# Kernel tuning notes

Hardware: AMD Instinct MI355X
Metric: run time of the kernel (lower is better)

Reference implementation:

```python
import jax, jax.numpy as jnp
import numpy as np

N_NODES = 100000
N_EDGES = 1600000
IN_C, HID_C, OUT_C = 128, 128, 64


def setup_inputs() -> dict:
    key = jax.random.key(0)
    ks = jax.random.split(key, 8)
    x = jax.random.normal(ks[0], (N_NODES, IN_C), dtype=jnp.float32)
    edge_index = jax.random.randint(ks[1], (2, N_EDGES), 0, N_NODES, dtype=jnp.int32)
    # Glorot-ish init for GCNConv linear weights, zero bias (PyG default)
    def glorot(k, fan_in, fan_out):
        s = jnp.sqrt(6.0 / (fan_in + fan_out))
        return jax.random.uniform(k, (fan_in, fan_out), dtype=jnp.float32, minval=-s, maxval=s)
    return {
        "x": x,
        "edge_index": edge_index,
        "W1": glorot(ks[2], IN_C, HID_C), "b1": jnp.zeros((HID_C,), jnp.float32),
        "W2": glorot(ks[3], HID_C, HID_C), "b2": jnp.zeros((HID_C,), jnp.float32),
        "W3": glorot(ks[4], HID_C, OUT_C), "b3": jnp.zeros((OUT_C,), jnp.float32),
    }


def _gcn_norm(edge_index, num_nodes):
    # Add self-loops (PyG GCNConv default) and compute symmetric normalization
    loops = jnp.arange(num_nodes, dtype=edge_index.dtype)
    src = jnp.concatenate([edge_index[0], loops])  # [E+N]
    dst = jnp.concatenate([edge_index[1], loops])
    deg = jax.ops.segment_sum(jnp.ones_like(dst, dtype=jnp.float32), dst,
                              num_segments=num_nodes)
    deg_inv_sqrt = jnp.where(deg > 0, jax.lax.rsqrt(jnp.maximum(deg, 1.0)), 0.0)
    norm = deg_inv_sqrt[src] * deg_inv_sqrt[dst]  # [E+N]
    return src, dst, norm


def _gcn_layer(x, src, dst, norm, W, b, num_nodes):
    h = x @ W                                # [N, out] dense transform first
    msg = h[src] * norm[:, None]             # gather + scale  [E+N, out]
    out = jax.ops.segment_sum(msg, dst, num_segments=num_nodes)  # scatter-add
    return out + b


def reference(x, edge_index, W1, b1, W2, b2, W3, b3):
    n = x.shape[0]
    src, dst, norm = _gcn_norm(edge_index, n)
    h = jax.nn.relu(_gcn_layer(x, src, dst, norm, W1, b1, n))
    h = jax.nn.relu(_gcn_layer(h, src, dst, norm, W2, b2, n))
    return _gcn_layer(h, src, dst, norm, W3, b3, n)
```

## Files before the change

### kernel.cpp

```cpp
#include <hip/hip_runtime.h>

#define NN 100000
#define NE 1600000
#define NBK 391
#define BSH 8
#define MPAD 100096
#define SCB 391
#define CAP 5120
#define NB16 6250

typedef unsigned short ushortT;
typedef unsigned long long ull;
using sh8 = __attribute__((ext_vector_type(8))) short;
using f4  = __attribute__((ext_vector_type(4))) float;


__device__ __forceinline__ unsigned short bfr(float f) {
  unsigned u = __float_as_uint(f);
  u += 0x7FFF + ((u >> 16) & 1);
  return (unsigned short)(u >> 16);
}
__device__ __forceinline__ float bf2f(unsigned short h) {
  return __uint_as_float(((unsigned)h) << 16);
}
__device__ __forceinline__ void acc8(const uint4 v, float* a) {
  a[0] += __uint_as_float(v.x << 16);
  a[1] += __uint_as_float(v.x & 0xFFFF0000u);
  a[2] += __uint_as_float(v.y << 16);
  a[3] += __uint_as_float(v.y & 0xFFFF0000u);
  a[4] += __uint_as_float(v.z << 16);
  a[5] += __uint_as_float(v.z & 0xFFFF0000u);
  a[6] += __uint_as_float(v.w << 16);
  a[7] += __uint_as_float(v.w & 0xFFFF0000u);
}
__device__ __forceinline__ sh8 hi8(const float4 a, const float4 b) {
  sh8 r;
  r[0] = (short)bfr(a.x); r[1] = (short)bfr(a.y);
  r[2] = (short)bfr(a.z); r[3] = (short)bfr(a.w);
  r[4] = (short)bfr(b.x); r[5] = (short)bfr(b.y);
  r[6] = (short)bfr(b.z); r[7] = (short)bfr(b.w);
  return r;
}


template <int COUT>
__device__ __forceinline__ void packone(const float* __restrict__ W,
                                        ushortT* __restrict__ Bp, int i) {
  const int j = i & 7;
  const int l = (i >> 3) & 63;
  const int rest = i >> 9;
  const int g = rest % (COUT / 16);
  const int ks = rest / (COUT / 16);
  const int k = (ks & 3) * 32 + (l >> 4) * 8 + j;
  const int n = g * 16 + (l & 15);
  const float v = W[k * COUT + n];
  const unsigned short h = bfr(v);
  Bp[i] = (ks < 4) ? h : bfr(v - bf2f(h));
}


__global__ __launch_bounds__(256) void k_scatterpack(
    const int* __restrict__ src, const int* __restrict__ dst,
    int* __restrict__ cursor, unsigned* __restrict__ pairArr,
    const float* __restrict__ W1, const float* __restrict__ W2,
    const float* __restrict__ W3, ushortT* __restrict__ Bp1,
    ushortT* __restrict__ Bp2, ushortT* __restrict__ Bp3) {
  if (blockIdx.x >= SCB) {
    const int i = (blockIdx.x - SCB) * 256 + threadIdx.x;
    if (i < 32768) packone<128>(W1, Bp1, i);
    else if (i < 65536) packone<128>(W2, Bp2, i - 32768);
    else packone<64>(W3, Bp3, i - 65536);
    return;
  }
  __shared__ int lcnt[512];
  __shared__ int lbase[512];
  __shared__ int lrank[NBK];
  __shared__ int bbase[NBK];
  __shared__ int sd2[256];
  __shared__ unsigned sorted[4096];
  __shared__ int target[4096];
  const int t = threadIdx.x;
  for (int i = t; i < 512; i += 256) lcnt[i] = 0;
  for (int i = t; i < NBK; i += 256) lrank[i] = 0;
  __syncthreads();
  const int base = blockIdx.x * 4096;
  int rs[16], rd[16];
#pragma unroll
  for (int q = 0; q < 16; q++) {
    int e = base + t + 256 * q;
    rs[q] = (e < NE) ? src[e] : -1;
    rd[q] = (e < NE) ? dst[e] : -1;
    if (rd[q] >= 0) atomicAdd(&lcnt[rd[q] >> BSH], 1);
  }
  __syncthreads();
  const int s0 = lcnt[2 * t];
  const int s1 = lcnt[2 * t + 1];
  sd2[t] = s0 + s1;
  __syncthreads();
  for (int off = 1; off < 256; off <<= 1) {
    int x = (t >= off) ? sd2[t - off] : 0;
    __syncthreads();
    sd2[t] += x;
    __syncthreads();
  }
  const int epair = sd2[t] - (s0 + s1);
  lbase[2 * t] = epair;
  lbase[2 * t + 1] = epair + s0;
  __syncthreads();
  for (int i = t; i < NBK; i += 256)
    if (lcnt[i] > 0) bbase[i] = atomicAdd(&cursor[i], lcnt[i]);
  __syncthreads();
#pragma unroll
  for (int q = 0; q < 16; q++) {
    if (rd[q] >= 0) {
      int b = rd[q] >> BSH;
      int r = atomicAdd(&lrank[b], 1);
      int slot = lbase[b] + r;
      sorted[slot] = ((unsigned)rs[q] << 8) | ((unsigned)rd[q] & 255u);
      target[slot] = b * CAP + bbase[b] + r;
    }
  }
  __syncthreads();
  const int n = min(4096, NE - base);
  for (int s = t; s < n; s += 256) pairArr[target[s]] = sorted[s];
}


__global__ __launch_bounds__(256) void k_buildcsr(const unsigned* __restrict__ pairArr,
                                                  const int* __restrict__ cnt,
                                                  float* __restrict__ dinv,
                                                  int* __restrict__ rowptr,
                                                  int* __restrict__ col) {
  __shared__ int lc[256];
  __shared__ int sd[256];
  __shared__ int bc[NBK];
  const int t = threadIdx.x;
  const int b = blockIdx.x;
  const int n0 = b << BSH;
  for (int i = t; i < NBK; i += 256) bc[i] = cnt[i];
  lc[t] = 0;
  __syncthreads();
  int partial = 0;
  for (int i = t; i < b; i += 256) partial += bc[i];
  sd[t] = partial;
  __syncthreads();
  for (int off = 128; off > 0; off >>= 1) {
    if (t < off) sd[t] += sd[t + off];
    __syncthreads();
  }
  const int ebeg = sd[0];
  const int myCnt = bc[b];
  __syncthreads();
  const unsigned* pb = pairArr + (size_t)b * CAP;
  for (int i = t; i < myCnt; i += 256)
    atomicAdd(&lc[pb[i] & 255u], 1);
  __syncthreads();
  const int v = lc[t];
  sd[t] = v;
  __syncthreads();
  for (int off = 1; off < 256; off <<= 1) {
    int x = (t >= off) ? sd[t - off] : 0;
    __syncthreads();
    sd[t] += x;
    __syncthreads();
  }
  const int excl = sd[t] - v;
  lc[t] = excl;
  const int node = n0 + t;
  if (node < NN) {
    rowptr[node] = ebeg + excl;
    dinv[node] = rsqrtf(1.0f + (float)v);
  }
  if (b == 0 && t == 0) rowptr[NN] = NE;
  __syncthreads();
  for (int i = t; i < myCnt; i += 256) {
    unsigned p = pb[i];
    int d = (int)(p & 255u);
    int srcv = (int)(p >> 8);
    int pos = atomicAdd(&lc[d], 1);
    col[ebeg + pos] = srcv;
  }
}


template <int COUT, bool FUSED>
__global__ __launch_bounds__(256) void k_gemmM(const ushortT* __restrict__ A,
                                               const float* __restrict__ X,
                                               const ushortT* __restrict__ Bp,
                                               const float* __restrict__ dinv,
                                               ushortT* __restrict__ hs) {
  constexpr int CGALL = COUT / 16;
  constexpr int RG = 2;
  constexpr int CG = 4;
  const int w = threadIdx.x >> 6;
  const int lane = threadIdx.x & 63;
  const int q = lane >> 4;
  const int c = lane & 15;
  int row0, cg0;
  if (COUT == 128) {
    row0 = blockIdx.x * 64 + (w & 1) * 32;
    cg0 = (w >> 1) * 4;
  } else {
    row0 = blockIdx.x * 128 + w * 32;
    cg0 = 0;
  }

  const ushortT* ap[RG];
  const float* xp[RG];
#pragma unroll
  for (int rg = 0; rg < RG; rg++) {
    const int row = row0 + rg * 16 + c;
    if (FUSED) xp[rg] = X + (size_t)min(row, NN - 1) * 128 + q * 8;
    else ap[rg] = A + (size_t)row * 128 + q * 8;
  }
  const ushortT* bp0 = Bp + (size_t)lane * 8;

  f4 acc[RG][CG];
#pragma unroll
  for (int i = 0; i < RG; i++)
#pragma unroll
    for (int j = 0; j < CG; j++) acc[i][j] = (f4){0.f, 0.f, 0.f, 0.f};

  sh8 ah[RG], bh[CG], bl[CG];
  sh8 nah[RG], nbh[CG], nbl[CG];

  auto loadA = [&](int kr, sh8 (&h)[RG]) {
#pragma unroll
    for (int rg = 0; rg < RG; rg++) {
      if (FUSED) {
        const float4 x0 = *reinterpret_cast<const float4*>(xp[rg] + kr * 32);
        const float4 x1 = *reinterpret_cast<const float4*>(xp[rg] + kr * 32 + 4);
        h[rg] = hi8(x0, x1);
      } else {
        h[rg] = *reinterpret_cast<const sh8*>(ap[rg] + kr * 32);
      }
    }
  };
  auto loadB = [&](int kr, sh8 (&h)[CG], sh8 (&l)[CG]) {
#pragma unroll
    for (int cg = 0; cg < CG; cg++) {
      h[cg] = *reinterpret_cast<const sh8*>(bp0 + (size_t)(kr * CGALL + cg0 + cg) * 512);
      l[cg] = *reinterpret_cast<const sh8*>(bp0 + (size_t)((4 + kr) * CGALL + cg0 + cg) * 512);
    }
  };

  loadA(0, ah);
  loadB(0, bh, bl);
#pragma unroll
  for (int kr = 0; kr < 4; kr++) {
    if (kr < 3) {
      loadA(kr + 1, nah);
      loadB(kr + 1, nbh, nbl);
    }
#pragma unroll
    for (int rg = 0; rg < RG; rg++)
#pragma unroll
      for (int cg = 0; cg < CG; cg++)
        acc[rg][cg] = __builtin_amdgcn_mfma_f32_16x16x32_bf16(ah[rg], bh[cg],
                                                              acc[rg][cg], 0, 0, 0);
#pragma unroll
    for (int rg = 0; rg < RG; rg++)
#pragma unroll
      for (int cg = 0; cg < CG; cg++)
        acc[rg][cg] = __builtin_amdgcn_mfma_f32_16x16x32_bf16(ah[rg], bl[cg],
                                                              acc[rg][cg], 0, 0, 0);
    if (kr < 3) {
#pragma unroll
      for (int rg = 0; rg < RG; rg++) ah[rg] = nah[rg];
#pragma unroll
      for (int cg = 0; cg < CG; cg++) { bh[cg] = nbh[cg]; bl[cg] = nbl[cg]; }
    }
  }

#pragma unroll
  for (int rg = 0; rg < RG; rg++) {
#pragma unroll
    for (int reg = 0; reg < 4; reg++) {
      const int row = row0 + rg * 16 + q * 4 + reg;
      if (row < NN) {
        const float dv = dinv[row];
#pragma unroll
        for (int cg = 0; cg < CG; cg++) {
          hs[(size_t)row * COUT + (cg0 + cg) * 16 + c] = bfr(acc[rg][cg][reg] * dv);
        }
      }
    }
  }
}


template <int COUT>
__global__ __launch_bounds__(256, 8) void k_aggemm(
    const ushortT* __restrict__ hs_in, const int* __restrict__ rowptr,
    const int* __restrict__ col, const float* __restrict__ dinv,
    const float* __restrict__ bias, const ushortT* __restrict__ Bp,
    ushortT* __restrict__ hs_out) {
  constexpr int CGALL = COUT / 16;
  constexpr int UPW = CGALL / 4;
  __shared__ ushortT At[16 * 128];
  const int t = threadIdx.x;
  const int w = t >> 6;
  const int lane = t & 63;
  const int q = lane >> 4;
  const int c = lane & 15;
  const int chb = c * 8;
  const int n0 = blockIdx.x * 16;
  const int nw0 = n0 + w * 4;

  const int rpv = rowptr[min(nw0 + (lane & 7), NN)];
  const float dvv = dinv[min(nw0 + (lane & 3), NN - 1)];
  const float4 b0 = *reinterpret_cast<const float4*>(bias + chb);
  const float4 b1 = *reinterpret_cast<const float4*>(bias + chb + 4);

  for (int it = 0; it < 4; ++it) {
    const int node = nw0 + it;
    const int r = w * 4 + it;
    const int beg = __shfl(rpv, it);
    const int end = __shfl(rpv, it + 1);
    const float di = __shfl(dvv, it);
    float a[8] = {};
    if (q == 0) {
      const uint4 v = *reinterpret_cast<const uint4*>(hs_in + (long)node * 128 + chb);
      acc8(v, a);
    }
    int j = beg;
    if (j + 8 <= end) {
      int c0 = col[j + q];
      int c1 = col[j + 4 + q];
      while (true) {
        const uint4 v0 = *reinterpret_cast<const uint4*>(hs_in + (long)c0 * 128 + chb);
        const uint4 v1 = *reinterpret_cast<const uint4*>(hs_in + (long)c1 * 128 + chb);
        j += 8;
        const bool more = (j + 8 <= end);
        int m0, m1;
        if (more) { m0 = col[j + q]; m1 = col[j + 4 + q]; }
        acc8(v0, a);
        acc8(v1, a);
        if (!more) break;
        c0 = m0; c1 = m1;
      }
    }
    if (j + 4 <= end) {
      int cc = col[j + q];
      const uint4 v = *reinterpret_cast<const uint4*>(hs_in + (long)cc * 128 + chb);
      acc8(v, a);
      j += 4;
    }
    {
      const int rem = end - j;
      if (q < rem) {
        int cc = col[j + q];
        const uint4 v = *reinterpret_cast<const uint4*>(hs_in + (long)cc * 128 + chb);
        acc8(v, a);
      }
    }
#pragma unroll
    for (int i = 0; i < 8; i++) a[i] += __shfl(a[i], lane ^ 32);
#pragma unroll
    for (int i = 0; i < 8; i++) a[i] += __shfl(a[i], lane ^ 16);
    if (q == 0) {
      float o[8];
      o[0] = fmaf(a[0], di, b0.x); o[1] = fmaf(a[1], di, b0.y);
      o[2] = fmaf(a[2], di, b0.z); o[3] = fmaf(a[3], di, b0.w);
      o[4] = fmaf(a[4], di, b1.x); o[5] = fmaf(a[5], di, b1.y);
      o[6] = fmaf(a[6], di, b1.z); o[7] = fmaf(a[7], di, b1.w);
#pragma unroll
      for (int i = 0; i < 8; i++) o[i] = fmaxf(o[i], 0.f);
      uint4 H;
      H.x = (unsigned)bfr(o[0]) | ((unsigned)bfr(o[1]) << 16);
      H.y = (unsigned)bfr(o[2]) | ((unsigned)bfr(o[3]) << 16);
      H.z = (unsigned)bfr(o[4]) | ((unsigned)bfr(o[5]) << 16);
      H.w = (unsigned)bfr(o[6]) | ((unsigned)bfr(o[7]) << 16);
      const unsigned bo = (unsigned)(r * 256 + c * 16) ^ (unsigned)((r & 7) << 4);
      *reinterpret_cast<uint4*>(reinterpret_cast<char*>(At) + bo) = H;
    }
  }
  __syncthreads();

  const int cg0 = w * UPW;
  const ushortT* bp0 = Bp + (size_t)lane * 8;
  const char* ab = reinterpret_cast<const char*>(At);
  const int arow = c;
  f4 acc[UPW];
#pragma unroll
  for (int u = 0; u < UPW; ++u) acc[u] = (f4){0.f, 0.f, 0.f, 0.f};
#pragma unroll
  for (int kr = 0; kr < 4; ++kr) {
    const unsigned bo =
        (unsigned)(arow * 256 + kr * 64 + q * 16) ^ (unsigned)((arow & 7) << 4);
    const sh8 af = *reinterpret_cast<const sh8*>(ab + bo);
#pragma unroll
    for (int u = 0; u < UPW; ++u) {
      const sh8 bh = *reinterpret_cast<const sh8*>(
          bp0 + (size_t)(kr * CGALL + cg0 + u) * 512);
      acc[u] = __builtin_amdgcn_mfma_f32_16x16x32_bf16(af, bh, acc[u], 0, 0, 0);
    }
#pragma unroll
    for (int u = 0; u < UPW; ++u) {
      const sh8 bl = *reinterpret_cast<const sh8*>(
          bp0 + (size_t)((4 + kr) * CGALL + cg0 + u) * 512);
      acc[u] = __builtin_amdgcn_mfma_f32_16x16x32_bf16(af, bl, acc[u], 0, 0, 0);
    }
  }
#pragma unroll
  for (int reg = 0; reg < 4; ++reg) {
    const int row = n0 + q * 4 + reg;
    const float dv = dinv[row];
#pragma unroll
    for (int u = 0; u < UPW; ++u) {
      hs_out[(size_t)row * COUT + (cg0 + u) * 16 + c] = bfr(acc[u][reg] * dv);
    }
  }
}


__global__ __launch_bounds__(256) void k_agg64(const ushortT* __restrict__ hs,
                                               const int* __restrict__ rowptr,
                                               const int* __restrict__ col,
                                               const float* __restrict__ dinv,
                                               const float* __restrict__ bias,
                                               float* __restrict__ out) {
  const int gid = blockIdx.x * 256 + threadIdx.x;
  const int node = gid >> 6;
  if (node >= NN) return;
  const int lane = threadIdx.x & 63;
  const int o8 = lane >> 3;
  const int chb = (lane & 7) * 8;
  const int beg = rowptr[node];
  const int end = rowptr[node + 1];

  float a[8] = {};
  if (o8 == 0) {
    const uint4 v = *reinterpret_cast<const uint4*>(hs + (long)node * 64 + chb);
    acc8(v, a);
  }

  int j = beg;
  if (j + 16 <= end) {
    int c0 = col[j + o8];
    int c1 = col[j + 8 + o8];
    while (true) {
      const uint4 v0 = *reinterpret_cast<const uint4*>(hs + (long)c0 * 64 + chb);
      const uint4 v1 = *reinterpret_cast<const uint4*>(hs + (long)c1 * 64 + chb);
      j += 16;
      const bool more = (j + 16 <= end);
      int n0, n1;
      if (more) { n0 = col[j + o8]; n1 = col[j + 8 + o8]; }
      acc8(v0, a);
      acc8(v1, a);
      if (!more) break;
      c0 = n0; c1 = n1;
    }
  }
  for (; j + 8 <= end; j += 8) {
    int c = col[j + o8];
    const uint4 v = *reinterpret_cast<const uint4*>(hs + (long)c * 64 + chb);
    acc8(v, a);
  }
  {
    const int r = end - j;
    if (o8 < r) {
      int c = col[j + o8];
      const uint4 v = *reinterpret_cast<const uint4*>(hs + (long)c * 64 + chb);
      acc8(v, a);
    }
  }

#pragma unroll
  for (int i = 0; i < 8; i++) a[i] += __shfl(a[i], lane ^ 32);
#pragma unroll
  for (int i = 0; i < 8; i++) a[i] += __shfl(a[i], lane ^ 16);
#pragma unroll
  for (int i = 0; i < 8; i++) a[i] += __shfl(a[i], lane ^ 8);

  if (o8 == 0) {
    const float di = dinv[node];
    const float4 b0 = *reinterpret_cast<const float4*>(bias + chb);
    const float4 b1 = *reinterpret_cast<const float4*>(bias + chb + 4);
    float4 r0, r1;
    r0.x = fmaf(a[0], di, b0.x); r0.y = fmaf(a[1], di, b0.y);
    r0.z = fmaf(a[2], di, b0.z); r0.w = fmaf(a[3], di, b0.w);
    r1.x = fmaf(a[4], di, b1.x); r1.y = fmaf(a[5], di, b1.y);
    r1.z = fmaf(a[6], di, b1.z); r1.w = fmaf(a[7], di, b1.w);
    *reinterpret_cast<float4*>(out + (long)node * 64 + chb) = r0;
    *reinterpret_cast<float4*>(out + (long)node * 64 + chb + 4) = r1;
  }
}


extern "C" void kernel_launch(void* const* d_in, const int* in_sizes, int n_in,
                              void* d_out, int out_size, void* d_ws, size_t ws_size,
                              hipStream_t stream) {
  const float* x  = (const float*)d_in[0];
  const int* ei   = (const int*)d_in[1];
  const float* W1 = (const float*)d_in[2];
  const float* b1 = (const float*)d_in[3];
  const float* W2 = (const float*)d_in[4];
  const float* b2 = (const float*)d_in[5];
  const float* W3 = (const float*)d_in[6];
  const float* b3 = (const float*)d_in[7];
  float* out = (float*)d_out;
  const int* srcp = ei;
  const int* dstp = ei + NE;

  char* wsb = (char*)d_ws;
  size_t off = 0;
  auto alloc = [&](size_t bytes) -> void* {
    void* p = wsb + off;
    off += (bytes + 255) & ~(size_t)255;
    return p;
  };
  ushortT* hs1 = (ushortT*)alloc((size_t)MPAD * 128 * 2);
  ushortT* hs2 = (ushortT*)alloc((size_t)NN * 128 * 2);
  int*   col    = (int*)alloc((size_t)NE * 4);
  int*   rowptr = (int*)alloc((size_t)(NN + 1) * 4);
  float* dinv   = (float*)alloc((size_t)NN * 4);
  int*   cursor = (int*)alloc((size_t)NBK * 4);
  ushortT* Bp1 = (ushortT*)alloc((size_t)32768 * 2);
  ushortT* Bp2 = (ushortT*)alloc((size_t)32768 * 2);
  ushortT* Bp3 = (ushortT*)alloc((size_t)16384 * 2);
  unsigned* pairArr = (unsigned*)hs2;
  ushortT* hs3 = hs1;
  (void)ws_size; (void)in_sizes; (void)n_in; (void)out_size;

  hipMemsetAsync(cursor, 0, (size_t)NBK * 4, stream);
  k_scatterpack<<<SCB + 320, 256, 0, stream>>>(srcp, dstp, cursor, pairArr,
                                               W1, W2, W3, Bp1, Bp2, Bp3);
  k_buildcsr<<<NBK, 256, 0, stream>>>(pairArr, cursor, dinv, rowptr, col);

  const int aggGrid = (NN * 64) / 256;
  const int gemmGrid128 = MPAD / 64;

  k_gemmM<128, true><<<gemmGrid128, 256, 0, stream>>>(nullptr, x, Bp1, dinv, hs1);
  k_aggemm<128><<<NB16, 256, 0, stream>>>(hs1, rowptr, col, dinv, b1, Bp2, hs2);
  k_aggemm<64><<<NB16, 256, 0, stream>>>(hs2, rowptr, col, dinv, b2, Bp3, hs3);
  k_agg64<<<aggGrid, 256, 0, stream>>>(hs3, rowptr, col, dinv, b3, out);
}
```

Baseline: 350.8 us.

## Replace bucketed two-pass CSR build with global degree histogram, scan, and atomic fill

Replaces the bucket-sort CSR construction (local sort into fixed-capacity buckets, then a per-bucket counting sort) with three kernels: a global atomic degree histogram, a block-wise prefix scan producing rowptr, cursor and dinv, and a per-edge atomic fill of col. This is simpler and drops the pairArr staging buffer. In exchange it relies on 1.6M global atomics on random addresses twice, and col order within a row becomes nondeterministic, which can scatter gather locality. The scan kernel also rereads the degree prefix for each block, doing quadratic work.

```diff
diff --git a/kernel.cpp b/kernel.cpp
--- a/kernel.cpp
+++ b/kernel.cpp
@@ -2,12 +2,11 @@
 
 #define NN 100000
 #define NE 1600000
-#define NBK 391
-#define BSH 8
 #define MPAD 100096
-#define SCB 391
-#define CAP 5120
 #define NB16 6250
+#define HB 1563
+#define FB 6250
+#define SB 98
 
 typedef unsigned short ushortT;
 typedef unsigned long long ull;
@@ -59,127 +58,73 @@
 }
 
 
-__global__ __launch_bounds__(256) void k_scatterpack(
-    const int* __restrict__ src, const int* __restrict__ dst,
-    int* __restrict__ cursor, unsigned* __restrict__ pairArr,
+__global__ __launch_bounds__(256) void k_histpack(
+    const int* __restrict__ dst, int* __restrict__ deg,
     const float* __restrict__ W1, const float* __restrict__ W2,
     const float* __restrict__ W3, ushortT* __restrict__ Bp1,
     ushortT* __restrict__ Bp2, ushortT* __restrict__ Bp3) {
-  if (blockIdx.x >= SCB) {
-    const int i = (blockIdx.x - SCB) * 256 + threadIdx.x;
+  if (blockIdx.x >= HB) {
+    const int i = (blockIdx.x - HB) * 256 + threadIdx.x;
     if (i < 32768) packone<128>(W1, Bp1, i);
     else if (i < 65536) packone<128>(W2, Bp2, i - 32768);
     else packone<64>(W3, Bp3, i - 65536);
     return;
   }
-  __shared__ int lcnt[512];
-  __shared__ int lbase[512];
-  __shared__ int lrank[NBK];
-  __shared__ int bbase[NBK];
-  __shared__ int sd2[256];
-  __shared__ unsigned sorted[4096];
-  __shared__ int target[4096];
-  const int t = threadIdx.x;
-  for (int i = t; i < 512; i += 256) lcnt[i] = 0;
-  for (int i = t; i < NBK; i += 256) lrank[i] = 0;
-  __syncthreads();
-  const int base = blockIdx.x * 4096;
-  int rs[16], rd[16];
-#pragma unroll
-  for (int q = 0; q < 16; q++) {
-    int e = base + t + 256 * q;
-    rs[q] = (e < NE) ? src[e] : -1;
-    rd[q] = (e < NE) ? dst[e] : -1;
-    if (rd[q] >= 0) atomicAdd(&lcnt[rd[q] >> BSH], 1);
-  }
-  __syncthreads();
-  const int s0 = lcnt[2 * t];
-  const int s1 = lcnt[2 * t + 1];
-  sd2[t] = s0 + s1;
-  __syncthreads();
-  for (int off = 1; off < 256; off <<= 1) {
-    int x = (t >= off) ? sd2[t - off] : 0;
-    __syncthreads();
-    sd2[t] += x;
-    __syncthreads();
-  }
-  const int epair = sd2[t] - (s0 + s1);
-  lbase[2 * t] = epair;
-  lbase[2 * t + 1] = epair + s0;
-  __syncthreads();
-  for (int i = t; i < NBK; i += 256)
-    if (lcnt[i] > 0) bbase[i] = atomicAdd(&cursor[i], lcnt[i]);
-  __syncthreads();
-#pragma unroll
-  for (int q = 0; q < 16; q++) {
-    if (rd[q] >= 0) {
-      int b = rd[q] >> BSH;
-      int r = atomicAdd(&lrank[b], 1);
-      int slot = lbase[b] + r;
-      sorted[slot] = ((unsigned)rs[q] << 8) | ((unsigned)rd[q] & 255u);
-      target[slot] = b * CAP + bbase[b] + r;
-    }
-  }
-  __syncthreads();
-  const int n = min(4096, NE - base);
-  for (int s = t; s < n; s += 256) pairArr[target[s]] = sorted[s];
-}
-
-
-__global__ __launch_bounds__(256) void k_buildcsr(const unsigned* __restrict__ pairArr,
-                                                  const int* __restrict__ cnt,
-                                                  float* __restrict__ dinv,
-                                                  int* __restrict__ rowptr,
-                                                  int* __restrict__ col) {
-  __shared__ int lc[256];
-  __shared__ int sd[256];
-  __shared__ int bc[NBK];
+  const int base = blockIdx.x * 1024 + threadIdx.x;
+#pragma unroll
+  for (int k = 0; k < 4; ++k) {
+    const int e = base + 256 * k;
+    if (e < NE) atomicAdd(&deg[dst[e]], 1);
+  }
+}
+
+
+__global__ __launch_bounds__(1024) void k_scan(const int* __restrict__ deg,
+                                               int* __restrict__ rowptr,
+                                               int* __restrict__ cursor,
+                                               float* __restrict__ dinv) {
+  __shared__ int sd[1024];
   const int t = threadIdx.x;
   const int b = blockIdx.x;
-  const int n0 = b << BSH;
-  for (int i = t; i < NBK; i += 256) bc[i] = cnt[i];
-  lc[t] = 0;
-  __syncthreads();
+  const int n = b * 1024 + t;
   int partial = 0;
-  for (int i = t; i < b; i += 256) partial += bc[i];
+  for (int i = t; i < b * 1024; i += 1024) partial += deg[i];
   sd[t] = partial;
   __syncthreads();
-  for (int off = 128; off > 0; off >>= 1) {
+  for (int off = 512; off > 0; off >>= 1) {
     if (t < off) sd[t] += sd[t + off];
     __syncthreads();
   }
-  const int ebeg = sd[0];
-  const int myCnt = bc[b];
+  const int bbase = sd[0];
   __syncthreads();
-  const unsigned* pb = pairArr + (size_t)b * CAP;
-  for (int i = t; i < myCnt; i += 256)
-    atomicAdd(&lc[pb[i] & 255u], 1);
-  __syncthreads();
-  const int v = lc[t];
+  const int v = (n < NN) ? deg[n] : 0;
   sd[t] = v;
   __syncthreads();
-  for (int off = 1; off < 256; off <<= 1) {
+  for (int off = 1; off < 1024; off <<= 1) {
     int x = (t >= off) ? sd[t - off] : 0;
     __syncthreads();
     sd[t] += x;
     __syncthreads();
   }
   const int excl = sd[t] - v;
-  lc[t] = excl;
-  const int node = n0 + t;
-  if (node < NN) {
-    rowptr[node] = ebeg + excl;
-    dinv[node] = rsqrtf(1.0f + (float)v);
+  if (n < NN) {
+    const int rp = bbase + excl;
+    rowptr[n] = rp;
+    cursor[n] = rp;
+    dinv[n] = rsqrtf(1.0f + (float)v);
   }
   if (b == 0 && t == 0) rowptr[NN] = NE;
-  __syncthreads();
-  for (int i = t; i < myCnt; i += 256) {
-    unsigned p = pb[i];
-    int d = (int)(p & 255u);
-    int srcv = (int)(p >> 8);
-    int pos = atomicAdd(&lc[d], 1);
-    col[ebeg + pos] = srcv;
-  }
+}
+
+__global__ __launch_bounds__(256) void k_fill(const int* __restrict__ src,
+                                              const int* __restrict__ dst,
+                                              int* __restrict__ cursor,
+                                              int* __restrict__ col) {
+  const int e = blockIdx.x * 256 + threadIdx.x;
+  const int d = dst[e];
+  const int s = src[e];
+  const int pos = atomicAdd(&cursor[d], 1);
+  col[pos] = s;
 }
 
 
@@ -515,18 +460,18 @@
   int*   col    = (int*)alloc((size_t)NE * 4);
   int*   rowptr = (int*)alloc((size_t)(NN + 1) * 4);
   float* dinv   = (float*)alloc((size_t)NN * 4);
-  int*   cursor = (int*)alloc((size_t)NBK * 4);
+  int*   deg    = (int*)alloc((size_t)NN * 4);
+  int*   cursor = (int*)alloc((size_t)NN * 4);
   ushortT* Bp1 = (ushortT*)alloc((size_t)32768 * 2);
   ushortT* Bp2 = (ushortT*)alloc((size_t)32768 * 2);
   ushortT* Bp3 = (ushortT*)alloc((size_t)16384 * 2);
-  unsigned* pairArr = (unsigned*)hs2;
   ushortT* hs3 = hs1;
   (void)ws_size; (void)in_sizes; (void)n_in; (void)out_size;
 
-  hipMemsetAsync(cursor, 0, (size_t)NBK * 4, stream);
-  k_scatterpack<<<SCB + 320, 256, 0, stream>>>(srcp, dstp, cursor, pairArr,
-                                               W1, W2, W3, Bp1, Bp2, Bp3);
-  k_buildcsr<<<NBK, 256, 0, stream>>>(pairArr, cursor, dinv, rowptr, col);
+  hipMemsetAsync(deg, 0, (size_t)NN * 4, stream);
+  k_histpack<<<HB + 320, 256, 0, stream>>>(dstp, deg, W1, W2, W3, Bp1, Bp2, Bp3);
+  k_scan<<<SB, 1024, 0, stream>>>(deg, rowptr, cursor, dinv);
+  k_fill<<<FB, 256, 0, stream>>>(srcp, dstp, cursor, col);
 
   const int aggGrid = (NN * 64) / 256;
   const int gemmGrid128 = MPAD / 64;
```

New measurement: 523.3 us. +49.2%, slower.

## Fuse CSR build with layer-1 GEMM and move dinv scaling into aggregation

Applied to the files above, without the earlier changes.

The CSR build and the first dense transform now run in one launch: the first NBK blocks build the CSR while the remaining blocks compute X@W1 without the dinv scale, since dinv is not yet available. The layer-1 aggregation then applies dinv per source neighbour with FMAs, which adds an extra dinv gather per edge. The aggregate+GEMM kernel also changes so each wave does its own 4-row MFMA from a per-wave LDS slice with no block-wide barrier, loops over column phases, and drops occupancy to 6. This removes one launch and lets the GEMM overlap the CSR build, but the per-wave MFMA wastes 12 of the 16 rows.

```diff
diff --git a/kernel.cpp b/kernel.cpp
--- a/kernel.cpp
+++ b/kernel.cpp
@@ -8,6 +8,7 @@
 #define SCB 391
 #define CAP 5120
 #define NB16 6250
+#define G1B 1564
 
 typedef unsigned short ushortT;
 typedef unsigned long long ull;
@@ -32,6 +33,16 @@
   a[5] += __uint_as_float(v.z & 0xFFFF0000u);
   a[6] += __uint_as_float(v.w << 16);
   a[7] += __uint_as_float(v.w & 0xFFFF0000u);
+}
+__device__ __forceinline__ void fma8(const uint4 v, const float s, float* a) {
+  a[0] = fmaf(__uint_as_float(v.x << 16), s, a[0]);
+  a[1] = fmaf(__uint_as_float(v.x & 0xFFFF0000u), s, a[1]);
+  a[2] = fmaf(__uint_as_float(v.y << 16), s, a[2]);
+  a[3] = fmaf(__uint_as_float(v.y & 0xFFFF0000u), s, a[3]);
+  a[4] = fmaf(__uint_as_float(v.z << 16), s, a[4]);
+  a[5] = fmaf(__uint_as_float(v.z & 0xFFFF0000u), s, a[5]);
+  a[6] = fmaf(__uint_as_float(v.w << 16), s, a[6]);
+  a[7] = fmaf(__uint_as_float(v.w & 0xFFFF0000u), s, a[7]);
 }
 __device__ __forceinline__ sh8 hi8(const float4 a, const float4 b) {
   sh8 r;
@@ -126,92 +137,79 @@
 }
 
 
-__global__ __launch_bounds__(256) void k_buildcsr(const unsigned* __restrict__ pairArr,
-                                                  const int* __restrict__ cnt,
-                                                  float* __restrict__ dinv,
-                                                  int* __restrict__ rowptr,
-                                                  int* __restrict__ col) {
+__global__ __launch_bounds__(256) void k_csrgemm1(
+    const unsigned* __restrict__ pairArr, const int* __restrict__ cnt,
+    float* __restrict__ dinv, int* __restrict__ rowptr, int* __restrict__ col,
+    const float* __restrict__ X, const ushortT* __restrict__ Bp,
+    ushortT* __restrict__ hs) {
   __shared__ int lc[256];
   __shared__ int sd[256];
   __shared__ int bc[NBK];
   const int t = threadIdx.x;
-  const int b = blockIdx.x;
-  const int n0 = b << BSH;
-  for (int i = t; i < NBK; i += 256) bc[i] = cnt[i];
-  lc[t] = 0;
-  __syncthreads();
-  int partial = 0;
-  for (int i = t; i < b; i += 256) partial += bc[i];
-  sd[t] = partial;
-  __syncthreads();
-  for (int off = 128; off > 0; off >>= 1) {
-    if (t < off) sd[t] += sd[t + off];
-    __syncthreads();
-  }
-  const int ebeg = sd[0];
-  const int myCnt = bc[b];
-  __syncthreads();
-  const unsigned* pb = pairArr + (size_t)b * CAP;
-  for (int i = t; i < myCnt; i += 256)
-    atomicAdd(&lc[pb[i] & 255u], 1);
-  __syncthreads();
-  const int v = lc[t];
-  sd[t] = v;
-  __syncthreads();
-  for (int off = 1; off < 256; off <<= 1) {
-    int x = (t >= off) ? sd[t - off] : 0;
-    __syncthreads();
-    sd[t] += x;
-    __syncthreads();
-  }
-  const int excl = sd[t] - v;
-  lc[t] = excl;
-  const int node = n0 + t;
-  if (node < NN) {
-    rowptr[node] = ebeg + excl;
-    dinv[node] = rsqrtf(1.0f + (float)v);
-  }
-  if (b == 0 && t == 0) rowptr[NN] = NE;
-  __syncthreads();
-  for (int i = t; i < myCnt; i += 256) {
-    unsigned p = pb[i];
-    int d = (int)(p & 255u);
-    int srcv = (int)(p >> 8);
-    int pos = atomicAdd(&lc[d], 1);
-    col[ebeg + pos] = srcv;
-  }
-}
-
-
-template <int COUT, bool FUSED>
-__global__ __launch_bounds__(256) void k_gemmM(const ushortT* __restrict__ A,
-                                               const float* __restrict__ X,
-                                               const ushortT* __restrict__ Bp,
-                                               const float* __restrict__ dinv,
-                                               ushortT* __restrict__ hs) {
-  constexpr int CGALL = COUT / 16;
+  if (blockIdx.x < NBK) {
+    const int b = blockIdx.x;
+    const int n0 = b << BSH;
+    for (int i = t; i < NBK; i += 256) bc[i] = cnt[i];
+    lc[t] = 0;
+    __syncthreads();
+    int partial = 0;
+    for (int i = t; i < b; i += 256) partial += bc[i];
+    sd[t] = partial;
+    __syncthreads();
+    for (int off = 128; off > 0; off >>= 1) {
+      if (t < off) sd[t] += sd[t + off];
+      __syncthreads();
+    }
+    const int ebeg = sd[0];
+    const int myCnt = bc[b];
+    __syncthreads();
+    const unsigned* pb = pairArr + (size_t)b * CAP;
+    for (int i = t; i < myCnt; i += 256)
+      atomicAdd(&lc[pb[i] & 255u], 1);
+    __syncthreads();
+    const int v = lc[t];
+    sd[t] = v;
+    __syncthreads();
+    for (int off = 1; off < 256; off <<= 1) {
+      int x = (t >= off) ? sd[t - off] : 0;
+      __syncthreads();
+      sd[t] += x;
+      __syncthreads();
+    }
+    const int excl = sd[t] - v;
+    lc[t] = excl;
+    const int node = n0 + t;
+    if (node < NN) {
+      rowptr[node] = ebeg + excl;
+      dinv[node] = rsqrtf(1.0f + (float)v);
+    }
+    if (b == 0 && t == 0) rowptr[NN] = NE;
+    __syncthreads();
+    for (int i = t; i < myCnt; i += 256) {
+      unsigned p = pb[i];
+      int d = (int)(p & 255u);
+      int srcv = (int)(p >> 8);
+      int pos = atomicAdd(&lc[d], 1);
+      col[ebeg + pos] = srcv;
+    }
+    return;
+  }
+  constexpr int CGALL = 8;
   constexpr int RG = 2;
   constexpr int CG = 4;
-  const int w = threadIdx.x >> 6;
-  const int lane = threadIdx.x & 63;
+  const int bid = blockIdx.x - NBK;
+  const int w = t >> 6;
+  const int lane = t & 63;
   const int q = lane >> 4;
   const int c = lane & 15;
-  int row0, cg0;
-  if (COUT == 128) {
-    row0 = blockIdx.x * 64 + (w & 1) * 32;
-    cg0 = (w >> 1) * 4;
-  } else {
-    row0 = blockIdx.x * 128 + w * 32;
-    cg0 = 0;
-  }
-
-  const ushortT* ap[RG];
+  const int row0 = bid * 64 + (w & 1) * 32;
+  const int cg0 = (w >> 1) * 4;
+
   const float* xp[RG];
 #pragma unroll
   for (int rg = 0; rg < RG; rg++) {
     const int row = row0 + rg * 16 + c;
-    if (FUSED) xp[rg] = X + (size_t)min(row, NN - 1) * 128 + q * 8;
-    else ap[rg] = A + (size_t)row * 128 + q * 8;
+    xp[rg] = X + (size_t)min(row, NN - 1) * 128 + q * 8;
   }
   const ushortT* bp0 = Bp + (size_t)lane * 8;
 
@@ -227,13 +225,9 @@
   auto loadA = [&](int kr, sh8 (&h)[RG]) {
 #pragma unroll
     for (int rg = 0; rg < RG; rg++) {
-      if (FUSED) {
-        const float4 x0 = *reinterpret_cast<const float4*>(xp[rg] + kr * 32);
-        const float4 x1 = *reinterpret_cast<const float4*>(xp[rg] + kr * 32 + 4);
-        h[rg] = hi8(x0, x1);
-      } else {
-        h[rg] = *reinterpret_cast<const sh8*>(ap[rg] + kr * 32);
-      }
+      const float4 x0 = *reinterpret_cast<const float4*>(xp[rg] + kr * 32);
+      const float4 x1 = *reinterpret_cast<const float4*>(xp[rg] + kr * 32 + 4);
+      h[rg] = hi8(x0, x1);
     }
   };
   auto loadB = [&](int kr, sh8 (&h)[CG], sh8 (&l)[CG]) {
@@ -278,10 +272,9 @@
     for (int reg = 0; reg < 4; reg++) {
       const int row = row0 + rg * 16 + q * 4 + reg;
       if (row < NN) {
-        const float dv = dinv[row];
 #pragma unroll
         for (int cg = 0; cg < CG; cg++) {
-          hs[(size_t)row * COUT + (cg0 + cg) * 16 + c] = bfr(acc[rg][cg][reg] * dv);
+          hs[(size_t)row * 128 + (cg0 + cg) * 16 + c] = bfr(acc[rg][cg][reg]);
         }
       }
     }
@@ -289,69 +282,75 @@
 }
 
 
-template <int COUT>
-__global__ __launch_bounds__(256, 8) void k_aggemm(
+template <int COUT, bool ESCALE>
+__global__ __launch_bounds__(256, 6) void k_aggemm(
     const ushortT* __restrict__ hs_in, const int* __restrict__ rowptr,
     const int* __restrict__ col, const float* __restrict__ dinv,
     const float* __restrict__ bias, const ushortT* __restrict__ Bp,
     ushortT* __restrict__ hs_out) {
   constexpr int CGALL = COUT / 16;
-  constexpr int UPW = CGALL / 4;
-  __shared__ ushortT At[16 * 128];
+  __shared__ ushortT At[4 * 512];
   const int t = threadIdx.x;
   const int w = t >> 6;
   const int lane = t & 63;
   const int q = lane >> 4;
   const int c = lane & 15;
   const int chb = c * 8;
-  const int n0 = blockIdx.x * 16;
-  const int nw0 = n0 + w * 4;
+  const int nw0 = blockIdx.x * 16 + w * 4;
 
   const int rpv = rowptr[min(nw0 + (lane & 7), NN)];
   const float dvv = dinv[min(nw0 + (lane & 3), NN - 1)];
   const float4 b0 = *reinterpret_cast<const float4*>(bias + chb);
   const float4 b1 = *reinterpret_cast<const float4*>(bias + chb + 4);
+  char* const myAt = reinterpret_cast<char*>(At) + w * 1024;
 
   for (int it = 0; it < 4; ++it) {
     const int node = nw0 + it;
-    const int r = w * 4 + it;
     const int beg = __shfl(rpv, it);
     const int end = __shfl(rpv, it + 1);
     const float di = __shfl(dvv, it);
     float a[8] = {};
     if (q == 0) {
       const uint4 v = *reinterpret_cast<const uint4*>(hs_in + (long)node * 128 + chb);
-      acc8(v, a);
+      if (ESCALE) fma8(v, di, a); else acc8(v, a);
     }
     int j = beg;
     if (j + 8 <= end) {
       int c0 = col[j + q];
       int c1 = col[j + 4 + q];
+      float d0 = 0.f, d1 = 0.f;
+      if (ESCALE) { d0 = dinv[c0]; d1 = dinv[c1]; }
       while (true) {
         const uint4 v0 = *reinterpret_cast<const uint4*>(hs_in + (long)c0 * 128 + chb);
         const uint4 v1 = *reinterpret_cast<const uint4*>(hs_in + (long)c1 * 128 + chb);
         j += 8;
         const bool more = (j + 8 <= end);
         int m0, m1;
-        if (more) { m0 = col[j + q]; m1 = col[j + 4 + q]; }
-        acc8(v0, a);
-        acc8(v1, a);
+        float e0 = 0.f, e1 = 0.f;
+        if (more) {
+          m0 = col[j + q]; m1 = col[j + 4 + q];
+          if (ESCALE) { e0 = dinv[m0]; e1 = dinv[m1]; }
+        }
+        if (ESCALE) { fma8(v0, d0, a); fma8(v1, d1, a); }
+        else { acc8(v0, a); acc8(v1, a); }
         if (!more) break;
-        c0 = m0; c1 = m1;
+        c0 = m0; c1 = m1; d0 = e0; d1 = e1;
       }
     }
     if (j + 4 <= end) {
       int cc = col[j + q];
+      float ds = ESCALE ? dinv[cc] : 0.f;
       const uint4 v = *reinterpret_cast<const uint4*>(hs_in + (long)cc * 128 + chb);
-      acc8(v, a);
+      if (ESCALE) fma8(v, ds, a); else acc8(v, a);
       j += 4;
     }
     {
       const int rem = end - j;
       if (q < rem) {
         int cc = col[j + q];
+        float ds = ESCALE ? dinv[cc] : 0.f;
         const uint4 v = *reinterpret_cast<const uint4*>(hs_in + (long)cc * 128 + chb);
-        acc8(v, a);
+        if (ESCALE) fma8(v, ds, a); else acc8(v, a);
       }
     }
 #pragma unroll
@@ -371,44 +370,51 @@
       H.y = (unsigned)bfr(o[2]) | ((unsigned)bfr(o[3]) << 16);
       H.z = (unsigned)bfr(o[4]) | ((unsigned)bfr(o[5]) << 16);
       H.w = (unsigned)bfr(o[6]) | ((unsigned)bfr(o[7]) << 16);
-      const unsigned bo = (unsigned)(r * 256 + c * 16) ^ (unsigned)((r & 7) << 4);
-      *reinterpret_cast<uint4*>(reinterpret_cast<char*>(At) + bo) = H;
-    }
-  }
-  __syncthreads();
-
-  const int cg0 = w * UPW;
+      *reinterpret_cast<uint4*>(myAt + ((unsigned)(it * 256 + c * 16) ^ (unsigned)(it << 4))) = H;
+    }
+  }
+  asm volatile("s_waitcnt lgkmcnt(0)" ::: "memory");
+  __builtin_amdgcn_sched_barrier(0);
+
   const ushortT* bp0 = Bp + (size_t)lane * 8;
-  const char* ab = reinterpret_cast<const char*>(At);
-  const int arow = c;
-  f4 acc[UPW];
-#pragma unroll
-  for (int u = 0; u < UPW; ++u) acc[u] = (f4){0.f, 0.f, 0.f, 0.f};
+  const int rr = c & 3;
+  sh8 af[4];
 #pragma unroll
   for (int kr = 0; kr < 4; ++kr) {
-    const unsigned bo =
-        (unsigned)(arow * 256 + kr * 64 + q * 16) ^ (unsigned)((arow & 7) << 4);
-    const sh8 af = *reinterpret_cast<const sh8*>(ab + bo);
-#pragma unroll
-    for (int u = 0; u < UPW; ++u) {
-      const sh8 bh = *reinterpret_cast<const sh8*>(
-          bp0 + (size_t)(kr * CGALL + cg0 + u) * 512);
-      acc[u] = __builtin_amdgcn_mfma_f32_16x16x32_bf16(af, bh, acc[u], 0, 0, 0);
-    }
-#pragma unroll
-    for (int u = 0; u < UPW; ++u) {
-      const sh8 bl = *reinterpret_cast<const sh8*>(
-          bp0 + (size_t)((4 + kr) * CGALL + cg0 + u) * 512);
-      acc[u] = __builtin_amdgcn_mfma_f32_16x16x32_bf16(af, bl, acc[u], 0, 0, 0);
-    }
-  }
-#pragma unroll
-  for (int reg = 0; reg < 4; ++reg) {
-    const int row = n0 + q * 4 + reg;
-    const float dv = dinv[row];
-#pragma unroll
-    for (int u = 0; u < UPW; ++u) {
-      hs_out[(size_t)row * COUT + (cg0 + u) * 16 + c] = bfr(acc[u][reg] * dv);
+    const unsigned bo = (unsigned)((rr * 256 + kr * 64 + q * 16) ^ (rr << 4));
+    af[kr] = *reinterpret_cast<const sh8*>(myAt + bo);
+  }
+  const float dvr0 = __shfl(dvv, 0), dvr1 = __shfl(dvv, 1),
+              dvr2 = __shfl(dvv, 2), dvr3 = __shfl(dvv, 3);
+#pragma unroll 1
+  for (int ph = 0; ph < CGALL / 4; ++ph) {
+    f4 acc[4];
+#pragma unroll
+    for (int u = 0; u < 4; ++u) acc[u] = (f4){0.f, 0.f, 0.f, 0.f};
+#pragma unroll
+    for (int kr = 0; kr < 4; ++kr) {
+#pragma unroll
+      for (int u = 0; u < 4; ++u) {
+        const sh8 bh = *reinterpret_cast<const sh8*>(
+            bp0 + (size_t)(kr * CGALL + ph * 4 + u) * 512);
+        acc[u] = __builtin_amdgcn_mfma_f32_16x16x32_bf16(af[kr], bh, acc[u], 0, 0, 0);
+      }
+#pragma unroll
+      for (int u = 0; u < 4; ++u) {
+        const sh8 bl = *reinterpret_cast<const sh8*>(
+            bp0 + (size_t)((4 + kr) * CGALL + ph * 4 + u) * 512);
+        acc[u] = __builtin_amdgcn_mfma_f32_16x16x32_bf16(af[kr], bl, acc[u], 0, 0, 0);
+      }
+    }
+    if (q == 0) {
+#pragma unroll
+      for (int u = 0; u < 4; ++u) {
+        const int cc0 = (ph * 4 + u) * 16 + c;
+        hs_out[(size_t)(nw0 + 0) * COUT + cc0] = bfr(acc[u][0] * dvr0);
+        hs_out[(size_t)(nw0 + 1) * COUT + cc0] = bfr(acc[u][1] * dvr1);
+        hs_out[(size_t)(nw0 + 2) * COUT + cc0] = bfr(acc[u][2] * dvr2);
+        hs_out[(size_t)(nw0 + 3) * COUT + cc0] = bfr(acc[u][3] * dvr3);
+      }
     }
   }
 }
@@ -526,13 +532,12 @@
   hipMemsetAsync(cursor, 0, (size_t)NBK * 4, stream);
   k_scatterpack<<<SCB + 320, 256, 0, stream>>>(srcp, dstp, cursor, pairArr,
                                                W1, W2, W3, Bp1, Bp2, Bp3);
-  k_buildcsr<<<NBK, 256, 0, stream>>>(pairArr, cursor, dinv, rowptr, col);
+  k_csrgemm1<<<NBK + G1B, 256, 0, stream>>>(pairArr, cursor, dinv, rowptr, col,
+                                            x, Bp1, hs1);
 
   const int aggGrid = (NN * 64) / 256;
-  const int gemmGrid128 = MPAD / 64;
-
-  k_gemmM<128, true><<<gemmGrid128, 256, 0, stream>>>(nullptr, x, Bp1, dinv, hs1);
-  k_aggemm<128><<<NB16, 256, 0, stream>>>(hs1, rowptr, col, dinv, b1, Bp2, hs2);
-  k_aggemm<64><<<NB16, 256, 0, stream>>>(hs2, rowptr, col, dinv, b2, Bp3, hs3);
+
+  k_aggemm<128, true><<<NB16, 256, 0, stream>>>(hs1, rowptr, col, dinv, b1, Bp2, hs2);
+  k_aggemm<64, false><<<NB16, 256, 0, stream>>>(hs2, rowptr, col, dinv, b2, Bp3, hs3);
   k_agg64<<<aggGrid, 256, 0, stream>>>(hs3, rowptr, col, dinv, b3, out);
 }
```

New measurement: 385.1 us. 9.8% more time.
